# Optimization experiments

Measured on AMD Instinct MI355X. Metric: run time of the kernel, lower is better.

## Reference

```python
import jax, jax.numpy as jnp
import numpy as np

N_NODES = 100000
N_EDGES = 600000
D_FEAT = 128
EDIM = 128
N_CLASSES = 10


def setup_inputs() -> dict:
    key = jax.random.key(0)
    k_h, k_eh, k_w, k_b, k_s, k_d = jax.random.split(key, 6)
    h = jax.random.normal(k_h, (N_NODES, D_FEAT), dtype=jnp.float32)
    edge_h = jax.random.normal(k_eh, (N_EDGES, 1, EDIM), dtype=jnp.float32)
    # Linear(in_features*2 + edim -> out_classes); torch stores weight as [out, in]
    W_w = jax.random.normal(k_w, (N_CLASSES, 2 * D_FEAT + EDIM), dtype=jnp.float32) * 0.05
    W_b = jax.random.normal(k_b, (N_CLASSES,), dtype=jnp.float32) * 0.05
    src = jax.random.randint(k_s, (N_EDGES,), 0, N_NODES, dtype=jnp.int64)
    dst = jax.random.randint(k_d, (N_EDGES,), 0, N_NODES, dtype=jnp.int64)
    return {"h": h, "edge_h": edge_h, "W_w": W_w, "W_b": W_b, "src": src, "dst": dst}


def reference(h, edge_h, W_w, W_b, src, dst):
    # edge-wise gather of src/dst node features
    h_u = h[src]                      # [E, D]
    h_v = h[dst]                      # [E, D]
    h_uv = edge_h.reshape(edge_h.shape[0], edge_h.shape[2])  # [E, edim]
    feat = jnp.concatenate([h_u, h_v, h_uv], axis=1)          # [E, 2D+edim]
    score = feat @ W_w.T + W_b                                 # [E, C]
    return score
```

## Files before the change

kernel.cpp:

```cpp
#include <hip/hip_runtime.h>


typedef __attribute__((ext_vector_type(8))) short short8;
typedef __attribute__((ext_vector_type(4))) float f32x4;

#define NC    10
#define TPW   4
#define NFRAG 12
#define FRAG_BYTES 12288

__device__ __forceinline__ unsigned short f2bf(float f) {
    unsigned u = __builtin_bit_cast(unsigned, f);
    u += 0x7FFFu + ((u >> 16) & 1u);
    return (unsigned short)(u >> 16);
}

__device__ __forceinline__ short8 cvt8(f32x4 a, f32x4 b) {
    short8 s;
    s[0]=(short)f2bf(a[0]); s[1]=(short)f2bf(a[1]);
    s[2]=(short)f2bf(a[2]); s[3]=(short)f2bf(a[3]);
    s[4]=(short)f2bf(b[0]); s[5]=(short)f2bf(b[1]);
    s[6]=(short)f2bf(b[2]); s[7]=(short)f2bf(b[3]);
    return s;
}

__global__ void build_wfrag(const float* __restrict__ Ww, short8* __restrict__ frag) {
    const int l = threadIdx.x;
    const int n = l & 15;
    const int q = l >> 4;
#pragma unroll
    for (int t = 0; t < NFRAG; ++t) {
        short8 b = (short8)0;
        if (n < NC) {
            const float* w = Ww + n * 384 + t * 32 + q * 8;
            b = cvt8(*(const f32x4*)w, *(const f32x4*)(w + 4));
        }
        frag[t * 64 + l] = b;
    }
}

__global__ __launch_bounds__(256) void cvt_h_kernel(
    const float* __restrict__ h, short8* __restrict__ hb, long n8) {
    const long i = (long)blockIdx.x * 256 + threadIdx.x;
    if (i < n8) {
        const f32x4 a = *(const f32x4*)(h + i * 8);
        const f32x4 b = *(const f32x4*)(h + i * 8 + 4);
        hb[i] = cvt8(a, b);
    }
}

#define LGF(v0,v1,v2,v3,v4,v5,v6,v7,p)          \
    v0 = *(const f32x4*)((p) + 0);              \
    v1 = *(const f32x4*)((p) + 4);              \
    v2 = *(const f32x4*)((p) + 32);             \
    v3 = *(const f32x4*)((p) + 36);             \
    v4 = *(const f32x4*)((p) + 64);             \
    v5 = *(const f32x4*)((p) + 68);             \
    v6 = *(const f32x4*)((p) + 96);             \
    v7 = *(const f32x4*)((p) + 100);

template<bool BF16H>
__global__ __launch_bounds__(64, 3) void mlp_edge_mfma(
    const float* __restrict__ h,
    const unsigned short* __restrict__ hb,
    const float* __restrict__ eh,
    const short8* __restrict__ frag,
    const float* __restrict__ Wb,
    const int*   __restrict__ src,
    const int*   __restrict__ dst,
    float* __restrict__ out,
    int E)
{
    const int l = threadIdx.x;
    const int n = l & 15;
    const int q = l >> 4;

    short8 bf[NFRAG];
#pragma unroll
    for (int t = 0; t < NFRAG; ++t) bf[t] = frag[t * 64 + l];
    const float bias = (n < NC) ? Wb[n] : 0.f;

    const long tile0 = (long)blockIdx.x * TPW;

#pragma unroll 1
    for (int tt = 0; tt < TPW; ++tt) {
        const long base = (tile0 + tt) * 16;
        if (base >= E) break;
        const long e  = base + n;
        const long ec = (e < E) ? e : (long)(E - 1);
        const int  sA = src[ec];
        const int  dA = dst[ec];
        const float* pe = eh + ec * 128 + q * 8;

        f32x4 acc = {0.f, 0.f, 0.f, 0.f};
        f32x4 z0,z1,z2,z3,z4,z5,z6,z7;

        if constexpr (BF16H) {
            const short8* ps = (const short8*)(hb + (size_t)sA * 128 + q * 8);
            const short8* pd = (const short8*)(hb + (size_t)dA * 128 + q * 8);
            short8 s0,s1,s2,s3, d0,d1,d2,d3;
            s0 = ps[0]; s1 = ps[4]; s2 = ps[8]; s3 = ps[12];
            d0 = pd[0]; d1 = pd[4]; d2 = pd[8]; d3 = pd[12];
            LGF(z0,z1,z2,z3,z4,z5,z6,z7, pe)
            acc = __builtin_amdgcn_mfma_f32_16x16x32_bf16(s0, bf[0], acc, 0,0,0);
            acc = __builtin_amdgcn_mfma_f32_16x16x32_bf16(s1, bf[1], acc, 0,0,0);
            acc = __builtin_amdgcn_mfma_f32_16x16x32_bf16(s2, bf[2], acc, 0,0,0);
            acc = __builtin_amdgcn_mfma_f32_16x16x32_bf16(s3, bf[3], acc, 0,0,0);
            acc = __builtin_amdgcn_mfma_f32_16x16x32_bf16(d0, bf[4], acc, 0,0,0);
            acc = __builtin_amdgcn_mfma_f32_16x16x32_bf16(d1, bf[5], acc, 0,0,0);
            acc = __builtin_amdgcn_mfma_f32_16x16x32_bf16(d2, bf[6], acc, 0,0,0);
            acc = __builtin_amdgcn_mfma_f32_16x16x32_bf16(d3, bf[7], acc, 0,0,0);
        } else {
            const float* ps = h + (long)sA * 128 + q * 8;
            const float* pd = h + (long)dA * 128 + q * 8;
            f32x4 x0,x1,x2,x3,x4,x5,x6,x7;
            f32x4 y0,y1,y2,y3,y4,y5,y6,y7;
            LGF(x0,x1,x2,x3,x4,x5,x6,x7, ps)
            LGF(y0,y1,y2,y3,y4,y5,y6,y7, pd)
            LGF(z0,z1,z2,z3,z4,z5,z6,z7, pe)
            acc = __builtin_amdgcn_mfma_f32_16x16x32_bf16(cvt8(x0,x1), bf[0], acc, 0,0,0);
            acc = __builtin_amdgcn_mfma_f32_16x16x32_bf16(cvt8(x2,x3), bf[1], acc, 0,0,0);
            acc = __builtin_amdgcn_mfma_f32_16x16x32_bf16(cvt8(x4,x5), bf[2], acc, 0,0,0);
            acc = __builtin_amdgcn_mfma_f32_16x16x32_bf16(cvt8(x6,x7), bf[3], acc, 0,0,0);
            acc = __builtin_amdgcn_mfma_f32_16x16x32_bf16(cvt8(y0,y1), bf[4], acc, 0,0,0);
            acc = __builtin_amdgcn_mfma_f32_16x16x32_bf16(cvt8(y2,y3), bf[5], acc, 0,0,0);
            acc = __builtin_amdgcn_mfma_f32_16x16x32_bf16(cvt8(y4,y5), bf[6], acc, 0,0,0);
            acc = __builtin_amdgcn_mfma_f32_16x16x32_bf16(cvt8(y6,y7), bf[7], acc, 0,0,0);
        }
        acc = __builtin_amdgcn_mfma_f32_16x16x32_bf16(cvt8(z0,z1), bf[8],  acc, 0,0,0);
        acc = __builtin_amdgcn_mfma_f32_16x16x32_bf16(cvt8(z2,z3), bf[9],  acc, 0,0,0);
        acc = __builtin_amdgcn_mfma_f32_16x16x32_bf16(cvt8(z4,z5), bf[10], acc, 0,0,0);
        acc = __builtin_amdgcn_mfma_f32_16x16x32_bf16(cvt8(z6,z7), bf[11], acc, 0,0,0);

        if (n < NC) {
#pragma unroll
            for (int r = 0; r < 4; ++r) {
                const long e2 = base + q * 4 + r;
                if (e2 < E) out[e2 * NC + n] = acc[r] + bias;
            }
        }
    }
}

extern "C" void kernel_launch(void* const* d_in, const int* in_sizes, int n_in,
                              void* d_out, int out_size, void* d_ws, size_t ws_size,
                              hipStream_t stream) {
    const float* h   = (const float*)d_in[0];
    const float* eh  = (const float*)d_in[1];
    const float* Ww  = (const float*)d_in[2];
    const float* Wb  = (const float*)d_in[3];
    const int*   src = (const int*)d_in[4];
    const int*   dst = (const int*)d_in[5];
    float* out = (float*)d_out;

    const int E    = in_sizes[4];
    const int N128 = in_sizes[0];

    short8* frag = (short8*)d_ws;
    build_wfrag<<<1, 64, 0, stream>>>(Ww, frag);

    const int edgesPerBlock = 16 * TPW;
    const int blocks = (E + edgesPerBlock - 1) / edgesPerBlock;

    const size_t need = (size_t)FRAG_BYTES + (size_t)N128 * 2;
    if (ws_size >= need) {
        unsigned short* hb = (unsigned short*)((char*)d_ws + FRAG_BYTES);
        const long n8 = (long)N128 / 8;
        cvt_h_kernel<<<(int)((n8 + 255) / 256), 256, 0, stream>>>(h, (short8*)hb, n8);
        mlp_edge_mfma<true><<<blocks, 64, 0, stream>>>(h, hb, eh, frag, Wb, src, dst, out, E);
    } else {
        mlp_edge_mfma<false><<<blocks, 64, 0, stream>>>(h, nullptr, eh, frag, Wb, src, dst, out, E);
    }
}
```

Baseline: 482.4 us.

## Precompute per-node projections and gather them instead of node features

Exploits linearity: a per-node pass computes h@W_src^T (+bias) and h@W_dst^T into padded 16-float tables, and the edge kernel gathers 10-float rows for src and dst instead of 128-element feature rows. Only the edge-feature term still uses MFMA per edge. This cuts random-gather traffic and edge-side MFMA work. In exchange it adds a node-level GEMM pass and per-lane scattered scalar loads from the tables.

```diff
diff --git a/kernel.cpp b/kernel.cpp
--- a/kernel.cpp
+++ b/kernel.cpp
@@ -8,6 +8,7 @@
 #define TPW   4
 #define NFRAG 12
 #define FRAG_BYTES 12288
+#define PSTRIDE 16
 
 __device__ __forceinline__ unsigned short f2bf(float f) {
     unsigned u = __builtin_bit_cast(unsigned, f);
@@ -36,16 +37,6 @@
             b = cvt8(*(const f32x4*)w, *(const f32x4*)(w + 4));
         }
         frag[t * 64 + l] = b;
-    }
-}
-
-__global__ __launch_bounds__(256) void cvt_h_kernel(
-    const float* __restrict__ h, short8* __restrict__ hb, long n8) {
-    const long i = (long)blockIdx.x * 256 + threadIdx.x;
-    if (i < n8) {
-        const f32x4 a = *(const f32x4*)(h + i * 8);
-        const f32x4 b = *(const f32x4*)(h + i * 8 + 4);
-        hb[i] = cvt8(a, b);
     }
 }
 
@@ -59,17 +50,118 @@
     v6 = *(const f32x4*)((p) + 96);             \
     v7 = *(const f32x4*)((p) + 100);
 
-template<bool BF16H>
-__global__ __launch_bounds__(64, 3) void mlp_edge_mfma(
-    const float* __restrict__ h,
-    const unsigned short* __restrict__ hb,
+__global__ __launch_bounds__(64) void build_ptab(
+    const float* __restrict__ h, const short8* __restrict__ frag,
+    const float* __restrict__ Wb, float* __restrict__ P1,
+    float* __restrict__ P2, int N)
+{
+    const int l = threadIdx.x;
+    const int n = l & 15;
+    const int q = l >> 4;
+    short8 bf[8];
+#pragma unroll
+    for (int t = 0; t < 8; ++t) bf[t] = frag[t * 64 + l];
+    const float bias = (n < NC) ? Wb[n] : 0.f;
+
+    const long base = (long)blockIdx.x * 16;
+    const long node = base + n;
+    const long ndc = (node < N) ? node : (long)(N - 1);
+    const float* ph = h + ndc * 128 + q * 8;
+
+    f32x4 x0,x1,x2,x3,x4,x5,x6,x7;
+    LGF(x0,x1,x2,x3,x4,x5,x6,x7, ph)
+    const short8 a0 = cvt8(x0,x1), a1 = cvt8(x2,x3);
+    const short8 a2 = cvt8(x4,x5), a3 = cvt8(x6,x7);
+
+    f32x4 acc1 = {0.f,0.f,0.f,0.f}, acc2 = {0.f,0.f,0.f,0.f};
+    acc1 = __builtin_amdgcn_mfma_f32_16x16x32_bf16(a0, bf[0], acc1, 0,0,0);
+    acc1 = __builtin_amdgcn_mfma_f32_16x16x32_bf16(a1, bf[1], acc1, 0,0,0);
+    acc1 = __builtin_amdgcn_mfma_f32_16x16x32_bf16(a2, bf[2], acc1, 0,0,0);
+    acc1 = __builtin_amdgcn_mfma_f32_16x16x32_bf16(a3, bf[3], acc1, 0,0,0);
+    acc2 = __builtin_amdgcn_mfma_f32_16x16x32_bf16(a0, bf[4], acc2, 0,0,0);
+    acc2 = __builtin_amdgcn_mfma_f32_16x16x32_bf16(a1, bf[5], acc2, 0,0,0);
+    acc2 = __builtin_amdgcn_mfma_f32_16x16x32_bf16(a2, bf[6], acc2, 0,0,0);
+    acc2 = __builtin_amdgcn_mfma_f32_16x16x32_bf16(a3, bf[7], acc2, 0,0,0);
+
+#pragma unroll
+    for (int r = 0; r < 4; ++r) {
+        const long nd = base + q * 4 + r;
+        if (nd < N) {
+            P1[nd * PSTRIDE + n] = acc1[r] + bias;
+            P2[nd * PSTRIDE + n] = acc2[r];
+        }
+    }
+}
+
+__global__ __launch_bounds__(64, 4) void mlp_edge_fused(
     const float* __restrict__ eh,
     const short8* __restrict__ frag,
-    const float* __restrict__ Wb,
+    const float* __restrict__ P1,
+    const float* __restrict__ P2,
     const int*   __restrict__ src,
     const int*   __restrict__ dst,
     float* __restrict__ out,
     int E)
+{
+    const int l = threadIdx.x;
+    const int n = l & 15;
+    const int q = l >> 4;
+
+    const short8 bf0 = frag[ 8 * 64 + l];
+    const short8 bf1 = frag[ 9 * 64 + l];
+    const short8 bf2 = frag[10 * 64 + l];
+    const short8 bf3 = frag[11 * 64 + l];
+    const int cn = (n < NC) ? n : 0;
+
+    const long tile0 = (long)blockIdx.x * TPW;
+
+#pragma unroll 1
+    for (int tt = 0; tt < TPW; ++tt) {
+        const long base = (tile0 + tt) * 16;
+        if (base >= E) break;
+        const long e  = base + n;
+        const long ec = (e < E) ? e : (long)(E - 1);
+        const float* pe = eh + ec * 128 + q * 8;
+
+        f32x4 z0,z1,z2,z3,z4,z5,z6,z7;
+        LGF(z0,z1,z2,z3,z4,z5,z6,z7, pe)
+
+        int s2[4], d2[4];
+#pragma unroll
+        for (int r = 0; r < 4; ++r) {
+            const long e2  = base + q * 4 + r;
+            const long e2c = (e2 < E) ? e2 : (long)(E - 1);
+            s2[r] = src[e2c];
+            d2[r] = dst[e2c];
+        }
+        float pv1[4], pv2[4];
+#pragma unroll
+        for (int r = 0; r < 4; ++r) {
+            pv1[r] = P1[(long)s2[r] * PSTRIDE + cn];
+            pv2[r] = P2[(long)d2[r] * PSTRIDE + cn];
+        }
+
+        f32x4 acc = {0.f, 0.f, 0.f, 0.f};
+        acc = __builtin_amdgcn_mfma_f32_16x16x32_bf16(cvt8(z0,z1), bf0, acc, 0,0,0);
+        acc = __builtin_amdgcn_mfma_f32_16x16x32_bf16(cvt8(z2,z3), bf1, acc, 0,0,0);
+        acc = __builtin_amdgcn_mfma_f32_16x16x32_bf16(cvt8(z4,z5), bf2, acc, 0,0,0);
+        acc = __builtin_amdgcn_mfma_f32_16x16x32_bf16(cvt8(z6,z7), bf3, acc, 0,0,0);
+
+        if (n < NC) {
+#pragma unroll
+            for (int r = 0; r < 4; ++r) {
+                const long e2 = base + q * 4 + r;
+                if (e2 < E) out[e2 * NC + n] = acc[r] + pv1[r] + pv2[r];
+            }
+        }
+    }
+}
+
+__global__ __launch_bounds__(64, 3) void mlp_edge_f32(
+    const float* __restrict__ h, const float* __restrict__ eh,
+    const short8* __restrict__ frag, const float* __restrict__ Wb,
+    const int* __restrict__ src, const int* __restrict__ dst,
+    float* __restrict__ out, int E)
 {
     const int l = threadIdx.x;
     const int n = l & 15;
@@ -91,42 +183,25 @@
         const int  sA = src[ec];
         const int  dA = dst[ec];
         const float* pe = eh + ec * 128 + q * 8;
+        const float* ps = h + (long)sA * 128 + q * 8;
+        const float* pd = h + (long)dA * 128 + q * 8;
+
+        f32x4 x0,x1,x2,x3,x4,x5,x6,x7;
+        f32x4 y0,y1,y2,y3,y4,y5,y6,y7;
+        f32x4 z0,z1,z2,z3,z4,z5,z6,z7;
+        LGF(x0,x1,x2,x3,x4,x5,x6,x7, ps)
+        LGF(y0,y1,y2,y3,y4,y5,y6,y7, pd)
+        LGF(z0,z1,z2,z3,z4,z5,z6,z7, pe)
 
         f32x4 acc = {0.f, 0.f, 0.f, 0.f};
-        f32x4 z0,z1,z2,z3,z4,z5,z6,z7;
-
-        if constexpr (BF16H) {
-            const short8* ps = (const short8*)(hb + (size_t)sA * 128 + q * 8);
-            const short8* pd = (const short8*)(hb + (size_t)dA * 128 + q * 8);
-            short8 s0,s1,s2,s3, d0,d1,d2,d3;
-            s0 = ps[0]; s1 = ps[4]; s2 = ps[8]; s3 = ps[12];
-            d0 = pd[0]; d1 = pd[4]; d2 = pd[8]; d3 = pd[12];
-            LGF(z0,z1,z2,z3,z4,z5,z6,z7, pe)
-            acc = __builtin_amdgcn_mfma_f32_16x16x32_bf16(s0, bf[0], acc, 0,0,0);
-            acc = __builtin_amdgcn_mfma_f32_16x16x32_bf16(s1, bf[1], acc, 0,0,0);
-            acc = __builtin_amdgcn_mfma_f32_16x16x32_bf16(s2, bf[2], acc, 0,0,0);
-            acc = __builtin_amdgcn_mfma_f32_16x16x32_bf16(s3, bf[3], acc, 0,0,0);
-            acc = __builtin_amdgcn_mfma_f32_16x16x32_bf16(d0, bf[4], acc, 0,0,0);
-            acc = __builtin_amdgcn_mfma_f32_16x16x32_bf16(d1, bf[5], acc, 0,0,0);
-            acc = __builtin_amdgcn_mfma_f32_16x16x32_bf16(d2, bf[6], acc, 0,0,0);
-            acc = __builtin_amdgcn_mfma_f32_16x16x32_bf16(d3, bf[7], acc, 0,0,0);
-        } else {
-            const float* ps = h + (long)sA * 128 + q * 8;
-            const float* pd = h + (long)dA * 128 + q * 8;
-            f32x4 x0,x1,x2,x3,x4,x5,x6,x7;
-            f32x4 y0,y1,y2,y3,y4,y5,y6,y7;
-            LGF(x0,x1,x2,x3,x4,x5,x6,x7, ps)
-            LGF(y0,y1,y2,y3,y4,y5,y6,y7, pd)
-            LGF(z0,z1,z2,z3,z4,z5,z6,z7, pe)
-            acc = __builtin_amdgcn_mfma_f32_16x16x32_bf16(cvt8(x0,x1), bf[0], acc, 0,0,0);
-            acc = __builtin_amdgcn_mfma_f32_16x16x32_bf16(cvt8(x2,x3), bf[1], acc, 0,0,0);
-            acc = __builtin_amdgcn_mfma_f32_16x16x32_bf16(cvt8(x4,x5), bf[2], acc, 0,0,0);
-            acc = __builtin_amdgcn_mfma_f32_16x16x32_bf16(cvt8(x6,x7), bf[3], acc, 0,0,0);
-            acc = __builtin_amdgcn_mfma_f32_16x16x32_bf16(cvt8(y0,y1), bf[4], acc, 0,0,0);
-            acc = __builtin_amdgcn_mfma_f32_16x16x32_bf16(cvt8(y2,y3), bf[5], acc, 0,0,0);
-            acc = __builtin_amdgcn_mfma_f32_16x16x32_bf16(cvt8(y4,y5), bf[6], acc, 0,0,0);
-            acc = __builtin_amdgcn_mfma_f32_16x16x32_bf16(cvt8(y6,y7), bf[7], acc, 0,0,0);
-        }
+        acc = __builtin_amdgcn_mfma_f32_16x16x32_bf16(cvt8(x0,x1), bf[0], acc, 0,0,0);
+        acc = __builtin_amdgcn_mfma_f32_16x16x32_bf16(cvt8(x2,x3), bf[1], acc, 0,0,0);
+        acc = __builtin_amdgcn_mfma_f32_16x16x32_bf16(cvt8(x4,x5), bf[2], acc, 0,0,0);
+        acc = __builtin_amdgcn_mfma_f32_16x16x32_bf16(cvt8(x6,x7), bf[3], acc, 0,0,0);
+        acc = __builtin_amdgcn_mfma_f32_16x16x32_bf16(cvt8(y0,y1), bf[4], acc, 0,0,0);
+        acc = __builtin_amdgcn_mfma_f32_16x16x32_bf16(cvt8(y2,y3), bf[5], acc, 0,0,0);
+        acc = __builtin_amdgcn_mfma_f32_16x16x32_bf16(cvt8(y4,y5), bf[6], acc, 0,0,0);
+        acc = __builtin_amdgcn_mfma_f32_16x16x32_bf16(cvt8(y6,y7), bf[7], acc, 0,0,0);
         acc = __builtin_amdgcn_mfma_f32_16x16x32_bf16(cvt8(z0,z1), bf[8],  acc, 0,0,0);
         acc = __builtin_amdgcn_mfma_f32_16x16x32_bf16(cvt8(z2,z3), bf[9],  acc, 0,0,0);
         acc = __builtin_amdgcn_mfma_f32_16x16x32_bf16(cvt8(z4,z5), bf[10], acc, 0,0,0);
@@ -155,6 +230,7 @@
 
     const int E    = in_sizes[4];
     const int N128 = in_sizes[0];
+    const int N    = N128 / 128;
 
     short8* frag = (short8*)d_ws;
     build_wfrag<<<1, 64, 0, stream>>>(Ww, frag);
@@ -162,13 +238,14 @@
     const int edgesPerBlock = 16 * TPW;
     const int blocks = (E + edgesPerBlock - 1) / edgesPerBlock;
 
-    const size_t need = (size_t)FRAG_BYTES + (size_t)N128 * 2;
+    const size_t pfloats = (size_t)N * PSTRIDE;
+    const size_t need = (size_t)FRAG_BYTES + 2 * pfloats * sizeof(float);
     if (ws_size >= need) {
-        unsigned short* hb = (unsigned short*)((char*)d_ws + FRAG_BYTES);
-        const long n8 = (long)N128 / 8;
-        cvt_h_kernel<<<(int)((n8 + 255) / 256), 256, 0, stream>>>(h, (short8*)hb, n8);
-        mlp_edge_mfma<true><<<blocks, 64, 0, stream>>>(h, hb, eh, frag, Wb, src, dst, out, E);
+        float* P1 = (float*)((char*)d_ws + FRAG_BYTES);
+        float* P2 = P1 + pfloats;
+        build_ptab<<<(N + 15) / 16, 64, 0, stream>>>(h, frag, Wb, P1, P2, N);
+        mlp_edge_fused<<<blocks, 64, 0, stream>>>(eh, frag, P1, P2, src, dst, out, E);
     } else {
-        mlp_edge_mfma<false><<<blocks, 64, 0, stream>>>(h, nullptr, eh, frag, Wb, src, dst, out, E);
-    }
-}
+        mlp_edge_f32<<<blocks, 64, 0, stream>>>(h, eh, frag, Wb, src, dst, out, E);
+    }
+}
```

Result: faster. 459.5 us (-4.8%).
